# Performance work log

Hardware: AMD Instinct MI355X
Metric: run time of the kernel (lower is better)

## Reference

```python
import jax, jax.numpy as jnp
import numpy as np

B, L, D = 2048, 128, 512


def setup_inputs() -> dict:
    key = jax.random.key(0)
    k1, k2, k3, k4 = jax.random.split(key, 4)
    a_t = jax.random.uniform(k1, (B, L), dtype=jnp.float32)
    a_t = a_t / jnp.sum(a_t, axis=1, keepdims=True)  # attention-like weights
    r_t = jax.random.uniform(k2, (B, 2), dtype=jnp.float32)
    r_t = r_t / jnp.sum(r_t, axis=1, keepdims=True)  # shift/stay probs
    input_embedding = jax.random.normal(k3, (B, L, D), dtype=jnp.float32)
    # binary float mask (1 = valid token, 0 = padded), matching original usage
    padded_mask = jnp.round(jax.random.uniform(k4, (B, L), dtype=jnp.float32))
    return {"a_t": a_t, "r_t": r_t, "input_embedding": input_embedding,
            "padded_mask": padded_mask, "step": 0}


def reference(a_t, r_t, input_embedding, padded_mask, step):
    # Banded width-2 stencil (the torch loop has no true recurrence:
    # new_a_t[:, i] depends only on a_t, never on new_a_t).
    # For i in 1..L-1:
    #   ws_i = a_t[:, i-1] * r_t[:, 1] + a_t[:, i] * r_t[:, 0]
    #   new_a_t[:, i-1] += (1 - mask[:, i]) * ws_i
    #   new_a_t[:, i]   += mask[:, i] * ws_i
    ws = a_t[:, :-1] * r_t[:, 1:2] + a_t[:, 1:] * r_t[:, 0:1]  # [B, L-1]
    m = padded_mask[:, 1:]                                      # [B, L-1]
    base = jnp.zeros_like(a_t).at[:, 0].set(a_t[:, 0] * r_t[:, 0])
    left = jnp.pad((1.0 - m) * ws, ((0, 0), (0, 1)))  # lands on i-1
    stay = jnp.pad(m * ws, ((0, 0), (1, 0)))          # lands on i
    new_a_t = base + left + stay                      # [B, L]
    output = jnp.einsum('bl,bld->bd', new_a_t, input_embedding)  # [B, D]
    return (output, new_a_t)
```

## Files before the change

kernel.cpp:

```cpp
#include <hip/hip_runtime.h>
#include <hip/hip_bf16.h>

#define NB 2048
#define NL 128
#define ND 512

__device__ __forceinline__ float bf2f(unsigned int u) {
    union { unsigned int i; float f; } x;
    x.i = u << 16;
    return x.f;
}

__global__ __launch_bounds__(256, 4) void sa_kernel(
    const void* __restrict__ a_t_v,
    const void* __restrict__ r_t_v,
    const void* __restrict__ ie_v,
    const void* __restrict__ mask_v,
    float* __restrict__ out)
{
    const int b = blockIdx.x;
    const int tid = threadIdx.x;

    __shared__ float aS[NL], mS[NL], wsS[NL], naS[NL];
    __shared__ float partial[4][ND];
    __shared__ int flagS;
    __shared__ float r01S[2];

    if (tid < 64) {
        const unsigned short* hus = (const unsigned short*)a_t_v;
        float sbf = bf2f(hus[2 * tid]) + bf2f(hus[2 * tid + 1]);
        #pragma unroll
        for (int off = 32; off; off >>= 1) sbf += __shfl_down(sbf, off);
        if (tid == 0) flagS = (fabsf(sbf - 1.0f) < 0.05f) ? 1 : 0;
    }
    __syncthreads();
    const int isbf = flagS;

    if (isbf) {
        const unsigned short* aus = (const unsigned short*)a_t_v + (size_t)b * NL;
        const unsigned short* mus = (const unsigned short*)mask_v + (size_t)b * NL;
        if (tid < NL) { aS[tid] = bf2f(aus[tid]); mS[tid] = bf2f(mus[tid]); }
        if (tid == 0) {
            const unsigned short* rus = (const unsigned short*)r_t_v + (size_t)b * 2;
            r01S[0] = bf2f(rus[0]); r01S[1] = bf2f(rus[1]);
        }
    } else {
        const float* af = (const float*)a_t_v + (size_t)b * NL;
        const float* mf = (const float*)mask_v + (size_t)b * NL;
        if (tid < NL) { aS[tid] = af[tid]; mS[tid] = mf[tid]; }
        if (tid == 0) {
            const float* rf = (const float*)r_t_v + (size_t)b * 2;
            r01S[0] = rf[0]; r01S[1] = rf[1];
        }
    }
    __syncthreads();
    const float r0 = r01S[0], r1 = r01S[1];

    if (tid < NL - 1) wsS[tid] = aS[tid] * r1 + aS[tid + 1] * r0;
    __syncthreads();

    if (tid < NL) {
        float v = (tid == 0) ? aS[0] * r0 : mS[tid] * wsS[tid - 1];
        if (tid < NL - 1) v += (1.0f - mS[tid + 1]) * wsS[tid];
        naS[tid] = v;
        out[(size_t)NB * ND + (size_t)b * NL + tid] = v;
    }
    __syncthreads();

    const int w = tid >> 6;
    const int c = tid & 63;
    float acc[8];
    #pragma unroll
    for (int j = 0; j < 8; ++j) acc[j] = 0.f;

    if (isbf) {
        const uint4* base = (const uint4*)((const unsigned short*)ie_v + (size_t)b * NL * ND);
        #pragma unroll 8
        for (int i = 0; i < 32; ++i) {
            const int l = w * 32 + i;
            const float na = naS[l];
            uint4 v = base[(size_t)l * (ND / 8) + c];
            acc[0] = fmaf(na, bf2f(v.x & 0xffffu), acc[0]);
            acc[1] = fmaf(na, bf2f(v.x >> 16),     acc[1]);
            acc[2] = fmaf(na, bf2f(v.y & 0xffffu), acc[2]);
            acc[3] = fmaf(na, bf2f(v.y >> 16),     acc[3]);
            acc[4] = fmaf(na, bf2f(v.z & 0xffffu), acc[4]);
            acc[5] = fmaf(na, bf2f(v.z >> 16),     acc[5]);
            acc[6] = fmaf(na, bf2f(v.w & 0xffffu), acc[6]);
            acc[7] = fmaf(na, bf2f(v.w >> 16),     acc[7]);
        }
    } else {
        const float4* base = (const float4*)((const float*)ie_v + (size_t)b * NL * ND);
        #pragma unroll 4
        for (int i = 0; i < 32; ++i) {
            const int l = w * 32 + i;
            const float na = naS[l];
            float4 v0 = base[(size_t)l * (ND / 4) + c];
            float4 v1 = base[(size_t)l * (ND / 4) + 64 + c];
            acc[0] = fmaf(na, v0.x, acc[0]);
            acc[1] = fmaf(na, v0.y, acc[1]);
            acc[2] = fmaf(na, v0.z, acc[2]);
            acc[3] = fmaf(na, v0.w, acc[3]);
            acc[4] = fmaf(na, v1.x, acc[4]);
            acc[5] = fmaf(na, v1.y, acc[5]);
            acc[6] = fmaf(na, v1.z, acc[6]);
            acc[7] = fmaf(na, v1.w, acc[7]);
        }
    }

    if (isbf) {
        #pragma unroll
        for (int j = 0; j < 8; ++j) partial[w][c * 8 + j] = acc[j];
    } else {
        #pragma unroll
        for (int j = 0; j < 4; ++j) partial[w][4 * c + j] = acc[j];
        #pragma unroll
        for (int j = 0; j < 4; ++j) partial[w][256 + 4 * c + j] = acc[4 + j];
    }
    __syncthreads();

    #pragma unroll
    for (int k = 0; k < 2; ++k) {
        const int d = tid + k * 256;
        float s = partial[0][d] + partial[1][d] + partial[2][d] + partial[3][d];
        out[(size_t)b * ND + d] = s;
    }
}

extern "C" void kernel_launch(void* const* d_in, const int* in_sizes, int n_in,
                              void* d_out, int out_size, void* d_ws, size_t ws_size,
                              hipStream_t stream) {
    (void)in_sizes; (void)n_in; (void)out_size; (void)d_ws; (void)ws_size;
    const void* a_t  = d_in[0];
    const void* r_t  = d_in[1];
    const void* ie   = d_in[2];
    const void* mask = d_in[3];
    sa_kernel<<<dim3(NB), dim3(256), 0, stream>>>(a_t, r_t, ie, mask, (float*)d_out);
}
```

Baseline: 682.4 us.

## Process four batches per 512-thread block with batched 16-deep independent loads

Each block now handles four batch rows with 512 threads, loading all per-row metadata at once and then looping over batches. Inside each batch, every wave issues 16 independent vector loads up front before accumulating, splitting the sequence across 8 waves instead of 4. This aims to increase memory-level parallelism for the bandwidth-bound weighted sum, at the cost of fewer blocks and extra barriers per batch iteration.

After: 674.3 us. No clear change (-1.2%).

```diff
diff --git a/kernel.cpp b/kernel.cpp
--- a/kernel.cpp
+++ b/kernel.cpp
@@ -4,6 +4,8 @@
 #define NB 2048
 #define NL 128
 #define ND 512
+#define BPB 4
+#define NBLK (NB / BPB)
 
 __device__ __forceinline__ float bf2f(unsigned int u) {
     union { unsigned int i; float f; } x;
@@ -11,20 +13,22 @@
     return x.f;
 }
 
-__global__ __launch_bounds__(256, 4) void sa_kernel(
+__global__ __launch_bounds__(512, 4) void sa_kernel(
     const void* __restrict__ a_t_v,
     const void* __restrict__ r_t_v,
     const void* __restrict__ ie_v,
     const void* __restrict__ mask_v,
     float* __restrict__ out)
 {
-    const int b = blockIdx.x;
     const int tid = threadIdx.x;
+    const int w = tid >> 6;
+    const int c = tid & 63;
+    const int b0 = blockIdx.x * BPB;
 
-    __shared__ float aS[NL], mS[NL], wsS[NL], naS[NL];
-    __shared__ float partial[4][ND];
+    __shared__ float aA[BPB][NL], mA[BPB][NL], wsA[BPB][NL], naA[BPB][NL];
+    __shared__ __align__(16) float partial[8][ND];
+    __shared__ float rA[BPB][2];
     __shared__ int flagS;
-    __shared__ float r01S[2];
 
     if (tid < 64) {
         const unsigned short* hus = (const unsigned short*)a_t_v;
@@ -36,94 +40,100 @@
     __syncthreads();
     const int isbf = flagS;
 
+    const int bb = tid >> 7;
+    const int l  = tid & (NL - 1);
     if (isbf) {
-        const unsigned short* aus = (const unsigned short*)a_t_v + (size_t)b * NL;
-        const unsigned short* mus = (const unsigned short*)mask_v + (size_t)b * NL;
-        if (tid < NL) { aS[tid] = bf2f(aus[tid]); mS[tid] = bf2f(mus[tid]); }
-        if (tid == 0) {
-            const unsigned short* rus = (const unsigned short*)r_t_v + (size_t)b * 2;
-            r01S[0] = bf2f(rus[0]); r01S[1] = bf2f(rus[1]);
+        const unsigned short* aus = (const unsigned short*)a_t_v  + (size_t)b0 * NL;
+        const unsigned short* mus = (const unsigned short*)mask_v + (size_t)b0 * NL;
+        aA[bb][l] = bf2f(aus[tid]);
+        mA[bb][l] = bf2f(mus[tid]);
+        if (tid < 2 * BPB) {
+            const unsigned short* rus = (const unsigned short*)r_t_v + (size_t)b0 * 2;
+            rA[tid >> 1][tid & 1] = bf2f(rus[tid]);
         }
     } else {
-        const float* af = (const float*)a_t_v + (size_t)b * NL;
-        const float* mf = (const float*)mask_v + (size_t)b * NL;
-        if (tid < NL) { aS[tid] = af[tid]; mS[tid] = mf[tid]; }
-        if (tid == 0) {
-            const float* rf = (const float*)r_t_v + (size_t)b * 2;
-            r01S[0] = rf[0]; r01S[1] = rf[1];
+        const float* af = (const float*)a_t_v  + (size_t)b0 * NL;
+        const float* mf = (const float*)mask_v + (size_t)b0 * NL;
+        aA[bb][l] = af[tid];
+        mA[bb][l] = mf[tid];
+        if (tid < 2 * BPB) {
+            const float* rf = (const float*)r_t_v + (size_t)b0 * 2;
+            rA[tid >> 1][tid & 1] = rf[tid];
         }
     }
     __syncthreads();
-    const float r0 = r01S[0], r1 = r01S[1];
 
-    if (tid < NL - 1) wsS[tid] = aS[tid] * r1 + aS[tid + 1] * r0;
+    if (l < NL - 1) wsA[bb][l] = aA[bb][l] * rA[bb][1] + aA[bb][l + 1] * rA[bb][0];
     __syncthreads();
 
-    if (tid < NL) {
-        float v = (tid == 0) ? aS[0] * r0 : mS[tid] * wsS[tid - 1];
-        if (tid < NL - 1) v += (1.0f - mS[tid + 1]) * wsS[tid];
-        naS[tid] = v;
-        out[(size_t)NB * ND + (size_t)b * NL + tid] = v;
+    {
+        float v = (l == 0) ? aA[bb][0] * rA[bb][0] : mA[bb][l] * wsA[bb][l - 1];
+        if (l < NL - 1) v += (1.0f - mA[bb][l + 1]) * wsA[bb][l];
+        naA[bb][l] = v;
+        out[(size_t)NB * ND + (size_t)b0 * NL + tid] = v;
     }
     __syncthreads();
 
-    const int w = tid >> 6;
-    const int c = tid & 63;
-    float acc[8];
-    #pragma unroll
-    for (int j = 0; j < 8; ++j) acc[j] = 0.f;
+    for (int b2 = 0; b2 < BPB; ++b2) {
+        const int batch = b0 + b2;
+        const float* naB = naA[b2];
+        float acc0 = 0.f, acc1 = 0.f, acc2 = 0.f, acc3 = 0.f;
+        float acc4 = 0.f, acc5 = 0.f, acc6 = 0.f, acc7 = 0.f;
 
-    if (isbf) {
-        const uint4* base = (const uint4*)((const unsigned short*)ie_v + (size_t)b * NL * ND);
-        #pragma unroll 8
-        for (int i = 0; i < 32; ++i) {
-            const int l = w * 32 + i;
-            const float na = naS[l];
-            uint4 v = base[(size_t)l * (ND / 8) + c];
-            acc[0] = fmaf(na, bf2f(v.x & 0xffffu), acc[0]);
-            acc[1] = fmaf(na, bf2f(v.x >> 16),     acc[1]);
-            acc[2] = fmaf(na, bf2f(v.y & 0xffffu), acc[2]);
-            acc[3] = fmaf(na, bf2f(v.y >> 16),     acc[3]);
-            acc[4] = fmaf(na, bf2f(v.z & 0xffffu), acc[4]);
-            acc[5] = fmaf(na, bf2f(v.z >> 16),     acc[5]);
-            acc[6] = fmaf(na, bf2f(v.w & 0xffffu), acc[6]);
-            acc[7] = fmaf(na, bf2f(v.w >> 16),     acc[7]);
+        if (isbf) {
+            const uint4* p = (const uint4*)((const unsigned short*)ie_v
+                             + (size_t)batch * NL * ND) + c;
+            uint4 q[16];
+            #pragma unroll
+            for (int k = 0; k < 16; ++k) q[k] = p[(size_t)(k * 8 + w) * (ND / 8)];
+            #pragma unroll
+            for (int k = 0; k < 16; ++k) {
+                const float na = naB[k * 8 + w];
+                acc0 = fmaf(na, bf2f(q[k].x & 0xffffu), acc0);
+                acc1 = fmaf(na, bf2f(q[k].x >> 16),     acc1);
+                acc2 = fmaf(na, bf2f(q[k].y & 0xffffu), acc2);
+                acc3 = fmaf(na, bf2f(q[k].y >> 16),     acc3);
+                acc4 = fmaf(na, bf2f(q[k].z & 0xffffu), acc4);
+                acc5 = fmaf(na, bf2f(q[k].z >> 16),     acc5);
+                acc6 = fmaf(na, bf2f(q[k].w & 0xffffu), acc6);
+                acc7 = fmaf(na, bf2f(q[k].w >> 16),     acc7);
+            }
+            *(float4*)&partial[w][c * 8]     = make_float4(acc0, acc1, acc2, acc3);
+            *(float4*)&partial[w][c * 8 + 4] = make_float4(acc4, acc5, acc6, acc7);
+        } else {
+            const float4* pf = (const float4*)((const float*)ie_v
+                               + (size_t)batch * NL * ND) + c;
+            float4 f[16];
+            #pragma unroll
+            for (int k = 0; k < 16; ++k) f[k] = pf[(size_t)(k * 8 + w) * (ND / 4)];
+            #pragma unroll
+            for (int k = 0; k < 16; ++k) {
+                const float na = naB[k * 8 + w];
+                acc0 = fmaf(na, f[k].x, acc0);
+                acc1 = fmaf(na, f[k].y, acc1);
+                acc2 = fmaf(na, f[k].z, acc2);
+                acc3 = fmaf(na, f[k].w, acc3);
+            }
+            #pragma unroll
+            for (int k = 0; k < 16; ++k) f[k] = pf[(size_t)(k * 8 + w) * (ND / 4) + 64];
+            #pragma unroll
+            for (int k = 0; k < 16; ++k) {
+                const float na = naB[k * 8 + w];
+                acc4 = fmaf(na, f[k].x, acc4);
+                acc5 = fmaf(na, f[k].y, acc5);
+                acc6 = fmaf(na, f[k].z, acc6);
+                acc7 = fmaf(na, f[k].w, acc7);
+            }
+            *(float4*)&partial[w][c * 4]       = make_float4(acc0, acc1, acc2, acc3);
+            *(float4*)&partial[w][256 + c * 4] = make_float4(acc4, acc5, acc6, acc7);
         }
-    } else {
-        const float4* base = (const float4*)((const float*)ie_v + (size_t)b * NL * ND);
-        #pragma unroll 4
-        for (int i = 0; i < 32; ++i) {
-            const int l = w * 32 + i;
-            const float na = naS[l];
-            float4 v0 = base[(size_t)l * (ND / 4) + c];
-            float4 v1 = base[(size_t)l * (ND / 4) + 64 + c];
-            acc[0] = fmaf(na, v0.x, acc[0]);
-            acc[1] = fmaf(na, v0.y, acc[1]);
-            acc[2] = fmaf(na, v0.z, acc[2]);
-            acc[3] = fmaf(na, v0.w, acc[3]);
-            acc[4] = fmaf(na, v1.x, acc[4]);
-            acc[5] = fmaf(na, v1.y, acc[5]);
-            acc[6] = fmaf(na, v1.z, acc[6]);
-            acc[7] = fmaf(na, v1.w, acc[7]);
+        __syncthreads();
+        {
+            float s = partial[0][tid] + partial[1][tid] + partial[2][tid] + partial[3][tid]
+                    + partial[4][tid] + partial[5][tid] + partial[6][tid] + partial[7][tid];
+            out[(size_t)batch * ND + tid] = s;
         }
-    }
-
-    if (isbf) {
-        #pragma unroll
-        for (int j = 0; j < 8; ++j) partial[w][c * 8 + j] = acc[j];
-    } else {
-        #pragma unroll
-        for (int j = 0; j < 4; ++j) partial[w][4 * c + j] = acc[j];
-        #pragma unroll
-        for (int j = 0; j < 4; ++j) partial[w][256 + 4 * c + j] = acc[4 + j];
-    }
-    __syncthreads();
-
-    #pragma unroll
-    for (int k = 0; k < 2; ++k) {
-        const int d = tid + k * 256;
-        float s = partial[0][d] + partial[1][d] + partial[2][d] + partial[3][d];
-        out[(size_t)b * ND + d] = s;
+        __syncthreads();
     }
 }
 
@@ -135,5 +145,5 @@
     const void* r_t  = d_in[1];
     const void* ie   = d_in[2];
     const void* mask = d_in[3];
-    sa_kernel<<<dim3(NB), dim3(256), 0, stream>>>(a_t, r_t, ie, mask, (float*)d_out);
+    sa_kernel<<<dim3(NBLK), dim3(512), 0, stream>>>(a_t, r_t, ie, mask, (float*)d_out);
 }
```
